# Kernel optimization log

Hardware: AMD Instinct MI355X
Metric: run time of the kernel (lower is better)

Reference implementation:

```python
import jax, jax.numpy as jnp
import numpy as np

NUM_HEADS = 16


def setup_inputs() -> dict:
    key = jax.random.key(0)
    k1, k2, k3 = jax.random.split(key, 3)
    S, B, H = 2048, 2, 1024
    hidden_states = jax.random.normal(k1, (S, B, H), dtype=jnp.float32)
    attention_mask = jnp.zeros((1, S, S), dtype=jnp.float32)
    W_qkv = jax.random.normal(k2, (3 * H, H), dtype=jnp.float32) * 0.02
    b_qkv = jax.random.normal(k3, (3 * H,), dtype=jnp.float32) * 0.02
    return {"hidden_states": hidden_states, "attention_mask": attention_mask,
            "W_qkv": W_qkv, "b_qkv": b_qkv}


def reference(hidden_states, attention_mask, W_qkv, b_qkv):
    # hidden_states: [S, B, H] (seq-first, megatron layout)
    S, B, H = hidden_states.shape
    nh = NUM_HEADS
    hph = H // nh
    norm_factor = jax.lax.rsqrt(jnp.float32(hph))

    # fused QKV projection: [S, B, 3H] -> [S, B, nh, 3*hph]
    qkv = hidden_states @ W_qkv.T + b_qkv
    qkv = qkv.reshape(S, B, nh, 3 * hph)
    q, k, v = jnp.split(qkv, 3, axis=3)  # each [S, B, nh, hph]

    # raw scores: (Q K^T) * rsqrt(hph), megatron layout [B*nh, Sq, Sk]
    scores = jnp.einsum('sbhd,tbhd->bhst', q, k) * norm_factor
    matmul_result = scores.reshape(B * nh, S, S)

    # exp-based unnormalized attention: exp(scores + additive mask), no softmax divide
    attention_probs = jnp.exp(matmul_result + attention_mask)  # [B*nh, S, S]

    # context: probs @ V -> [S, B, nh, hph] -> [S, B, H]
    probs_bh = attention_probs.reshape(B, nh, S, S)
    context = jnp.einsum('bhst,tbhd->sbhd', probs_bh, v)
    context_layer = context.reshape(S, B, H)
    return (context_layer, matmul_result, attention_probs)
```

## Files before the change

kernel.cpp:

```cpp
#include <hip/hip_runtime.h>
#include <hip/hip_bf16.h>

#define S_  2048
#define B_  2
#define H_  1024
#define NH_ 16
#define D_  64

typedef short s16x8 __attribute__((ext_vector_type(8)));
typedef float f32x4 __attribute__((ext_vector_type(4)));
typedef unsigned short u16;

__device__ __forceinline__ u16 f2bf(float f) {
    __hip_bfloat16 h = __float2bfloat16(f);
    union { __hip_bfloat16 h; u16 u; } c; c.h = h; return c.u;
}

#define GLOAD_LDS16(g, l) __builtin_amdgcn_global_load_lds( \
    (const __attribute__((address_space(1))) void*)(g),     \
    (__attribute__((address_space(3))) void*)(l), 16, 0, 0)

__global__ __launch_bounds__(256) void cast_bf16(
    const float* __restrict__ A, const float* __restrict__ W,
    u16* __restrict__ Ab, u16* __restrict__ Wb)
{
    size_t g = (size_t)blockIdx.x * 256 + threadIdx.x;
    const float* src; u16* dst;
    if (g < 524288) { src = A + g * 8; dst = Ab + g * 8; }
    else            { size_t h = g - 524288; src = W + h * 8; dst = Wb + h * 8; }
    f32x4 a = *(const f32x4*)src;
    f32x4 b = *(const f32x4*)(src + 4);
    ushort4 lo, hi;
    lo.x = f2bf(a[0]); lo.y = f2bf(a[1]); lo.z = f2bf(a[2]); lo.w = f2bf(a[3]);
    hi.x = f2bf(b[0]); hi.y = f2bf(b[1]); hi.z = f2bf(b[2]); hi.w = f2bf(b[3]);
    *(ushort4*)dst = lo; *(ushort4*)(dst + 4) = hi;
}

__global__ __launch_bounds__(256) void qkv_gemm(
    const u16* __restrict__ Ab, const u16* __restrict__ Wb,
    const float* __restrict__ bias,
    u16* __restrict__ Qb, u16* __restrict__ Kb, u16* __restrict__ Vt)
{
    __shared__ u16 As[128 * 64];
    __shared__ u16 Bs[128 * 64];

    const int tid  = threadIdx.x;
    const int lane = tid & 63;
    const int w    = tid >> 6;
    const int wm   = (w >> 1) * 64;
    const int wn   = (w & 1) * 64;
    const int l15  = lane & 15;
    const int lg   = lane >> 4;
    const int mBase = blockIdx.y * 128;
    const int nBase = blockIdx.x * 128;

    int rS[4], cS[4];
    #pragma unroll
    for (int i = 0; i < 4; ++i) {
        int n = (w * 4 + i) * 64 + lane;
        rS[i] = n >> 3;
        cS[i] = (n & 7) ^ (rS[i] & 7);
    }

    f32x4 acc[4][4] = {};

    for (int kt = 0; kt < 1024; kt += 64) {
        __syncthreads();
        const u16* ab = Ab + (size_t)mBase * 1024 + kt;
        const u16* wb = Wb + (size_t)nBase * 1024 + kt;
        #pragma unroll
        for (int i = 0; i < 4; ++i) {
            GLOAD_LDS16(ab + (size_t)rS[i] * 1024 + cS[i] * 8, As + (w * 4 + i) * 512);
            GLOAD_LDS16(wb + (size_t)rS[i] * 1024 + cS[i] * 8, Bs + (w * 4 + i) * 512);
        }
        __syncthreads();

        #pragma unroll
        for (int kk = 0; kk < 2; ++kk) {
            s16x8 af[4], bfr[4];
            #pragma unroll
            for (int mi = 0; mi < 4; ++mi) {
                int row = wm + mi * 16 + l15;
                int byte = (row * 128 + ((kk * 64 + lg * 16) ^ ((row & 7) << 4)));
                af[mi] = *(const s16x8*)((const char*)As + byte);
            }
            #pragma unroll
            for (int ni = 0; ni < 4; ++ni) {
                int row = wn + ni * 16 + l15;
                int byte = (row * 128 + ((kk * 64 + lg * 16) ^ ((row & 7) << 4)));
                bfr[ni] = *(const s16x8*)((const char*)Bs + byte);
            }
            #pragma unroll
            for (int mi = 0; mi < 4; ++mi)
                #pragma unroll
                for (int ni = 0; ni < 4; ++ni)
                    acc[mi][ni] = __builtin_amdgcn_mfma_f32_16x16x32_bf16(
                        af[mi], bfr[ni], acc[mi][ni], 0, 0, 0);
        }
    }

    #pragma unroll
    for (int ni = 0; ni < 4; ++ni) {
        int gn = nBase + wn + ni * 16 + l15;
        float bv = bias[gn];
        int h  = gn / 192;
        int r  = gn - h * 192;
        int c  = r >> 6;
        int dd = r & 63;
        #pragma unroll
        for (int mi = 0; mi < 4; ++mi) {
            #pragma unroll
            for (int j = 0; j < 4; ++j) {
                int m = mBase + wm + mi * 16 + lg * 4 + j;
                float val = acc[mi][ni][j] + bv;
                int s = m >> 1, b = m & 1;
                int bh = b * 16 + h;
                u16 o = f2bf(val);
                if (c == 0)      Qb[((size_t)bh * S_ + s) * 64 + dd] = o;
                else if (c == 1) Kb[((size_t)bh * S_ + s) * 64 + dd] = o;
                else             Vt[((size_t)bh * 64 + dd) * S_ + s] = o;
            }
        }
    }
}

__global__ __launch_bounds__(256, 4) void attn(
    const u16* __restrict__ Qb, const u16* __restrict__ Kb, const u16* __restrict__ Vt,
    const float* __restrict__ mask,
    float* __restrict__ ctx, float* __restrict__ scores, float* __restrict__ probs)
{
    __shared__ u16 Ks[2][64 * 64];
    __shared__ u16 Vs[2][64 * 64];
    __shared__ float SG[4][512];

    const int tid  = threadIdx.x;
    const int lane = tid & 63;
    const int w    = tid >> 6;
    const int l15  = lane & 15;
    const int lg   = lane >> 4;

    const int lin  = blockIdx.y * 32 + blockIdx.x;
    const int orig = (lin & 7) * 128 + (lin >> 3);
    const int bh   = orig >> 5;
    const int rowQ = (orig & 31) * 64 + w * 16;

    const int nK = (w * 2) * 64 + lane;
    const int rK0 = nK >> 3, cK0 = (nK & 7) ^ (rK0 & 7);
    const int nK1 = nK + 64;
    const int rK1 = nK1 >> 3, cK1 = (nK1 & 7) ^ (rK1 & 7);

    s16x8 qf[2];
    #pragma unroll
    for (int kk = 0; kk < 2; ++kk)
        qf[kk] = *(const s16x8*)(Qb + ((size_t)bh * S_ + rowQ + l15) * 64 + kk * 32 + lg * 8);

    f32x4 cacc[4] = {};

    auto stage = [&](int buf, int tt) {
        const u16* kbase = Kb + (size_t)bh * S_ * 64 + (size_t)tt * 64;
        const u16* vbase = Vt + (size_t)bh * 64 * S_ + tt;
        GLOAD_LDS16(kbase + (size_t)rK0 * 64 + cK0 * 8, &Ks[buf][(w * 2 + 0) * 512]);
        GLOAD_LDS16(kbase + (size_t)rK1 * 64 + cK1 * 8, &Ks[buf][(w * 2 + 1) * 512]);
        GLOAD_LDS16(vbase + (size_t)rK0 * S_ + cK0 * 8, &Vs[buf][(w * 2 + 0) * 512]);
        GLOAD_LDS16(vbase + (size_t)rK1 * S_ + cK1 * 8, &Vs[buf][(w * 2 + 1) * 512]);
    };

    stage(0, 0);
    __syncthreads();
    int cur = 0;

    const int q = rowQ + l15;
    const float* mrow = mask + (size_t)q * S_;

    const int rdq   = lane >> 3;
    const int rslot = lane & 7;
    const int s0 = (lg >> 1) * 4 + (lg & 1) * 2;
    const int pvbyteA = l15 * 128 + (((s0 + 0) * 16) ^ ((l15 & 7) << 4));
    const int pvbyteB = l15 * 128 + (((s0 + 1) * 16) ^ ((l15 & 7) << 4));

    for (int tt = 0; tt < S_; tt += 64) {
        if (tt + 64 < S_) stage(cur ^ 1, tt + 64);

        f32x4 mv[4];
        #pragma unroll
        for (int tb = 0; tb < 4; ++tb)
            mv[tb] = *(const f32x4*)(mrow + tt + tb * 16 + lg * 4);

        f32x4 sacc[4] = {};
        #pragma unroll
        for (int kk = 0; kk < 2; ++kk) {
            #pragma unroll
            for (int tb = 0; tb < 4; ++tb) {
                int row = tb * 16 + l15;
                int byte = (row * 128 + ((kk * 64 + lg * 16) ^ ((row & 7) << 4)));
                s16x8 kf = *(const s16x8*)((const char*)Ks[cur] + byte);
                sacc[tb] = __builtin_amdgcn_mfma_f32_16x16x32_bf16(
                    kf, qf[kk], sacc[tb], 0, 0, 0);
            }
        }

        #pragma unroll
        for (int kv = 0; kv < 2; ++kv) {
            f32x4 s4[2], p4[2];
            #pragma unroll
            for (int th = 0; th < 2; ++th) {
                int tb = kv * 2 + th;
                f32x4 sc = sacc[tb];
                s4[th][0] = sc[0] * 0.125f + mv[tb][0];
                s4[th][1] = sc[1] * 0.125f + mv[tb][1];
                s4[th][2] = sc[2] * 0.125f + mv[tb][2];
                s4[th][3] = sc[3] * 0.125f + mv[tb][3];
                int sbyte = l15 * 128 + (((th * 4 + lg) * 16) ^ ((l15 & 7) << 4));
                *(f32x4*)((char*)SG[w] + sbyte) = s4[th];
            }
            #pragma unroll
            for (int p = 0; p < 2; ++p) {
                int qq = p * 8 + rdq;
                int rbyte = qq * 128 + ((rslot * 16) ^ ((qq & 7) << 4));
                f32x4 v = *(const f32x4*)((const char*)SG[w] + rbyte);
                __builtin_nontemporal_store(v, (f32x4*)(scores +
                    (size_t)bh * S_ * S_ + (size_t)(rowQ + qq) * S_ + tt + kv * 32 + rslot * 4));
            }
            #pragma unroll
            for (int th = 0; th < 2; ++th) {
                p4[th][0] = __expf(s4[th][0]); p4[th][1] = __expf(s4[th][1]);
                p4[th][2] = __expf(s4[th][2]); p4[th][3] = __expf(s4[th][3]);
                int sbyte = l15 * 128 + (((th * 4 + lg) * 16) ^ ((l15 & 7) << 4));
                *(f32x4*)((char*)SG[w] + sbyte) = p4[th];
            }
            #pragma unroll
            for (int p = 0; p < 2; ++p) {
                int qq = p * 8 + rdq;
                int rbyte = qq * 128 + ((rslot * 16) ^ ((qq & 7) << 4));
                f32x4 v = *(const f32x4*)((const char*)SG[w] + rbyte);
                __builtin_nontemporal_store(v, (f32x4*)(probs +
                    (size_t)bh * S_ * S_ + (size_t)(rowQ + qq) * S_ + tt + kv * 32 + rslot * 4));
            }
            f32x4 ra = *(const f32x4*)((const char*)SG[w] + pvbyteA);
            f32x4 rb = *(const f32x4*)((const char*)SG[w] + pvbyteB);
            unsigned int w0, w1, w2, w3;
            asm("v_cvt_pk_bf16_f32 %0, %1, %2" : "=v"(w0) : "v"(ra[0]), "v"(ra[1]));
            asm("v_cvt_pk_bf16_f32 %0, %1, %2" : "=v"(w1) : "v"(ra[2]), "v"(ra[3]));
            asm("v_cvt_pk_bf16_f32 %0, %1, %2" : "=v"(w2) : "v"(rb[0]), "v"(rb[1]));
            asm("v_cvt_pk_bf16_f32 %0, %1, %2" : "=v"(w3) : "v"(rb[2]), "v"(rb[3]));
            union { unsigned int u[4]; s16x8 v; } pk;
            pk.u[0] = w0; pk.u[1] = w1; pk.u[2] = w2; pk.u[3] = w3;
            s16x8 pa = pk.v;
            #pragma unroll
            for (int db = 0; db < 4; ++db) {
                int row = db * 16 + l15;
                int byte = (row * 128 + ((kv * 64 + lg * 16) ^ ((row & 7) << 4)));
                s16x8 vb = *(const s16x8*)((const char*)Vs[cur] + byte);
                cacc[db] = __builtin_amdgcn_mfma_f32_16x16x32_bf16(
                    pa, vb, cacc[db], 0, 0, 0);
            }
        }

        asm volatile("s_waitcnt vmcnt(8) lgkmcnt(0)" ::: "memory");
        __builtin_amdgcn_s_barrier();
        cur ^= 1;
    }

    const int b = bh >> 4, h = bh & 15;
    #pragma unroll
    for (int db = 0; db < 4; ++db)
        #pragma unroll
        for (int j = 0; j < 4; ++j) {
            int srow = rowQ + lg * 4 + j;
            int dd = db * 16 + l15;
            __builtin_nontemporal_store(cacc[db][j],
                ctx + ((size_t)srow * B_ + b) * H_ + h * 64 + dd);
        }
}

extern "C" void kernel_launch(void* const* d_in, const int* in_sizes, int n_in,
                              void* d_out, int out_size, void* d_ws, size_t ws_size,
                              hipStream_t stream) {
    const float* hidden = (const float*)d_in[0];
    const float* mask   = (const float*)d_in[1];
    const float* W      = (const float*)d_in[2];
    const float* bias   = (const float*)d_in[3];

    u16* Qb = (u16*)d_ws;
    u16* Kb = Qb + 4194304;
    u16* Vt = Kb + 4194304;

    float* out    = (float*)d_out;
    float* ctx    = out;
    float* scores = out + 4194304;
    float* probs  = out + 138412032;

    u16* Ab = (u16*)scores;
    u16* Wb = Ab + 4194304;

    cast_bf16<<<dim3(3584), 256, 0, stream>>>(hidden, W, Ab, Wb);
    qkv_gemm<<<dim3(24, 32), 256, 0, stream>>>(Ab, Wb, bias, Qb, Kb, Vt);
    attn<<<dim3(32, 32), 256, 0, stream>>>(Qb, Kb, Vt, mask, ctx, scores, probs);
}
```

Measured before the change: 298.1 us.

## Double-buffer QKV GEMM LDS tiles to overlap global loads with MFMA

The QKV projection GEMM now uses two LDS buffers per operand and issues the async global-to-LDS loads for the next K tile before computing on the current one. Explicit vmcnt waits and raw s_barrier calls replace the two __syncthreads per iteration, so load latency is meant to hide behind the MFMA work. LDS use doubles to 64KB per block, which may reduce occupancy. Correctness depends on the hand-written vmcnt counts matching the eight loads issued per stage.

```diff
diff --git a/kernel.cpp b/kernel.cpp
--- a/kernel.cpp
+++ b/kernel.cpp
@@ -41,8 +41,8 @@
     const float* __restrict__ bias,
     u16* __restrict__ Qb, u16* __restrict__ Kb, u16* __restrict__ Vt)
 {
-    __shared__ u16 As[128 * 64];
-    __shared__ u16 Bs[128 * 64];
+    __shared__ u16 As[2][128 * 64];
+    __shared__ u16 Bs[2][128 * 64];
 
     const int tid  = threadIdx.x;
     const int lane = tid & 63;
@@ -62,18 +62,34 @@
         cS[i] = (n & 7) ^ (rS[i] & 7);
     }
 
-    f32x4 acc[4][4] = {};
-
-    for (int kt = 0; kt < 1024; kt += 64) {
-        __syncthreads();
+    auto stage = [&](int buf, int kt) {
         const u16* ab = Ab + (size_t)mBase * 1024 + kt;
         const u16* wb = Wb + (size_t)nBase * 1024 + kt;
         #pragma unroll
         for (int i = 0; i < 4; ++i) {
-            GLOAD_LDS16(ab + (size_t)rS[i] * 1024 + cS[i] * 8, As + (w * 4 + i) * 512);
-            GLOAD_LDS16(wb + (size_t)rS[i] * 1024 + cS[i] * 8, Bs + (w * 4 + i) * 512);
-        }
-        __syncthreads();
+            GLOAD_LDS16(ab + (size_t)rS[i] * 1024 + cS[i] * 8, &As[buf][(w * 4 + i) * 512]);
+            GLOAD_LDS16(wb + (size_t)rS[i] * 1024 + cS[i] * 8, &Bs[buf][(w * 4 + i) * 512]);
+        }
+    };
+
+    f32x4 acc[4][4] = {};
+
+    stage(0, 0);
+    __syncthreads();
+
+    for (int it = 0; it < 16; ++it) {
+        const int cur = it & 1;
+        const int kt  = it * 64;
+        if (it > 0)
+            __builtin_amdgcn_s_barrier();
+        if (it < 15) {
+            stage(cur ^ 1, kt + 64);
+            if (it > 0)
+                asm volatile("s_waitcnt vmcnt(8)" ::: "memory");
+        } else {
+            asm volatile("s_waitcnt vmcnt(0)" ::: "memory");
+        }
+        __builtin_amdgcn_s_barrier();
 
         #pragma unroll
         for (int kk = 0; kk < 2; ++kk) {
@@ -82,13 +98,13 @@
             for (int mi = 0; mi < 4; ++mi) {
                 int row = wm + mi * 16 + l15;
                 int byte = (row * 128 + ((kk * 64 + lg * 16) ^ ((row & 7) << 4)));
-                af[mi] = *(const s16x8*)((const char*)As + byte);
+                af[mi] = *(const s16x8*)((const char*)As[cur] + byte);
             }
             #pragma unroll
             for (int ni = 0; ni < 4; ++ni) {
                 int row = wn + ni * 16 + l15;
                 int byte = (row * 128 + ((kk * 64 + lg * 16) ^ ((row & 7) << 4)));
-                bfr[ni] = *(const s16x8*)((const char*)Bs + byte);
+                bfr[ni] = *(const s16x8*)((const char*)Bs[cur] + byte);
             }
             #pragma unroll
             for (int mi = 0; mi < 4; ++mi)
```

New measurement: 294.5 us. About the same (-1.2%).
